# Performance work log

Hardware: AMD Instinct MI355X
Metric: run time of the kernel (lower is better)

The kernel has to match this reference:

```python
import jax, jax.numpy as jnp
import numpy as np

SIDE_LEN = 128
RESOLUTION = 1.0  # Angstrom per pixel


def setup_inputs() -> dict:
    key = jax.random.key(0)
    k1, k2, k3 = jax.random.split(key, 3)
    B, A = 16, 20000
    # atom xyz coords in Angstrom, spread within the field of view (+/- 63.5 A)
    mol = jax.random.normal(k1, (B, A, 3), dtype=jnp.float32) * 20.0
    # per-atom Gaussian std in [0.5, 1.5) A (strictly positive)
    stds = jax.random.uniform(k2, (A,), dtype=jnp.float32) + 0.5
    # per-atom density (mass) in [0.5, 1.5)
    densities = jax.random.uniform(k3, (A,), dtype=jnp.float32) + 0.5
    return {"mol": mol, "stds": stds, "densities": densities}


def reference(mol, stds, densities):
    # Pixel-center coordinate grid, identical to torch.arange(-x_max, x_max+1e-5, res)
    x_max = (SIDE_LEN - 1) * RESOLUTION / 2
    coord = jnp.arange(-x_max, x_max + 1e-5, RESOLUTION, dtype=jnp.float32)  # (S,)
    var = stds * stds                              # (A,)
    neg_half_inv_var = (-0.5 / var)[None, :, None] # (1,A,1)
    # Separable Gaussian profiles: exp(-(coord - mu)^2 / (2 var))
    dx = coord[None, None, :] - mol[:, :, 0:1]     # (B,A,S) x-offsets
    dy = coord[None, None, :] - mol[:, :, 1:2]     # (B,A,S) y-offsets
    gx = jnp.exp(neg_half_inv_var * dx * dx)       # (B,A,W)
    gy = jnp.exp(neg_half_inv_var * dy * dy)       # (B,A,H)
    coef = densities / (2.0 * jnp.pi * var)        # (A,)
    # img[b,h,w] = sum_a coef_a * gy[b,a,h] * gx[b,a,w]  (batched matmul)
    img = jnp.einsum('bah,baw->bhw', gy * coef[None, :, None], gx)
    return img  # (B, SIDE_LEN, SIDE_LEN)
```

## Files before the change

### kernel.cpp

```cpp
#include <hip/hip_runtime.h>


#define S 128
#define NS 32
#define PER 640
#define BLOCK 1024
#define KC 32
#define GSTR 40

typedef _Float16 f16;
typedef _Float16 f16x2 __attribute__((ext_vector_type(2)));
typedef _Float16 f16x4 __attribute__((ext_vector_type(4)));
typedef _Float16 f16x8 __attribute__((ext_vector_type(8)));
typedef float floatx16 __attribute__((ext_vector_type(16)));

#if __has_builtin(__builtin_amdgcn_exp2f)
#define FAST_EXP2(x) __builtin_amdgcn_exp2f(x)
#else
#define FAST_EXP2(x) exp2f(x)
#endif
#if __has_builtin(__builtin_amdgcn_rcpf)
#define FAST_RCP(x) __builtin_amdgcn_rcpf(x)
#else
#define FAST_RCP(x) (1.0f / (x))
#endif

static __device__ __forceinline__ f16x2 PKRTZ(float a, float b) {
#if __has_builtin(__builtin_amdgcn_cvt_pkrtz)
    return __builtin_bit_cast(f16x2, __builtin_amdgcn_cvt_pkrtz(a, b));
#else
    return (f16x2){(f16)a, (f16)b};
#endif
}

union frag_u { f16x8 v; f16x4 q[2]; f16x2 h[4]; };
union half4_u { f16x4 q; f16x2 h[2]; };

struct SharedT {
    float4 sG[PER];
    f16 g[2][2][S * GSTR];
};

__global__ __launch_bounds__(BLOCK, 8) void k_proj(
    const float* __restrict__ mol,
    const float* __restrict__ stds,
    const float* __restrict__ dens,
    f16* __restrict__ part,
    int B, int A)
{
    __shared__ SharedT sh;

    const int ks   = blockIdx.x;
    const int b    = blockIdx.y;
    const int tid  = threadIdx.x;
    const int lane = tid & 63;
    const int wav  = tid >> 6;
    const int l31  = lane & 31;
    const int hi   = lane >> 5;

    const int a0  = ks * PER;
    const int a1  = min(a0 + PER, A);
    const int cnt = a1 - a0;

    for (int i = tid; i < cnt; i += BLOCK) {
        const int a = a0 + i;
        const size_t idx = (size_t)b * A + a;
        float x  = mol[idx * 3 + 0];
        float y  = mol[idx * 3 + 1];
        float v  = stds[a] * stds[a];
        float rv = FAST_RCP(v);
        float z  = -0.72134752044448f * rv;
        float w  = __log2f(dens[a] * 0.15915494309189535f * rv);
        sh.sG[i] = make_float4(x, y, z, w);
    }
    __syncthreads();

    const int nc = cnt >> 5;

    const int gaxis = wav >> 3;
    const int agrp  = wav & 7;
    const float c0  = (float)lane - 63.5f;

    const int arow = (wav >> 2) * 32 + l31;
    const int bcol = (wav & 3) * 32 + l31;
    const int koff = hi * 8;

    floatx16 acc = (floatx16){0.f};

    auto GEN_COMPUTE = [&](int c, half4_u& V0, half4_u& V1) {
        const float4* prm = &sh.sG[c * KC + agrp * 4];
#pragma unroll
        for (int i2 = 0; i2 < 2; ++i2) {
            float e0[2], e1[2];
#pragma unroll
            for (int u = 0; u < 2; ++u) {
                float4 p = prm[i2 * 2 + u];
                float mu = gaxis ? p.y : p.x;
                float wc = gaxis ? p.w : 0.0f;
                float d  = c0 - mu;
                float t  = p.z * d;
                float g0 = fmaf(t, d, wc);
                float g1 = fmaf(128.0f, t, fmaf(4096.0f, p.z, g0));
                e0[u] = FAST_EXP2(g0);
                e1[u] = FAST_EXP2(g1);
            }
            V0.h[i2] = PKRTZ(e0[0], e0[1]);
            V1.h[i2] = PKRTZ(e1[0], e1[1]);
        }
    };

#define STEP(P)                                                                \
    do {                                                                       \
        const f16* gy = sh.g[(P)][1];                                          \
        const f16* gx = sh.g[(P)][0];                                          \
        const bool gen = (c + 1 < nc);                                         \
        half4_u V0, V1;                                                        \
        if (gen) GEN_COMPUTE(c + 1, V0, V1);                                   \
        _Pragma("unroll")                                                      \
        for (int s = 0; s < 2; ++s) {                                          \
            frag_u Af, Bf;                                                     \
            Af.v = *(const f16x8*)(gy + arow * GSTR + s * 16 + koff);          \
            Bf.v = *(const f16x8*)(gx + bcol * GSTR + s * 16 + koff);          \
            acc = __builtin_amdgcn_mfma_f32_32x32x16_f16(Af.v, Bf.v, acc, 0, 0, 0); \
        }                                                                      \
        if (gen) {                                                             \
            f16* dst = &sh.g[(P) ^ 1][gaxis][lane * GSTR + agrp * 4];          \
            *(f16x4*)dst               = V0.q;                                 \
            *(f16x4*)(dst + 64 * GSTR) = V1.q;                                 \
        }                                                                      \
        __syncthreads();                                                       \
        ++c;                                                                   \
    } while (0)

    {
        half4_u V0, V1;
        GEN_COMPUTE(0, V0, V1);
        f16* dst = &sh.g[0][gaxis][lane * GSTR + agrp * 4];
        *(f16x4*)dst               = V0.q;
        *(f16x4*)(dst + 64 * GSTR) = V1.q;
    }
    __syncthreads();

    int c = 0;
    while (c + 2 <= nc) { STEP(0); STEP(1); }
    if (c < nc) STEP(0);
#undef STEP

    {
        f16* pq = part + ((size_t)(b * NS + ks)) * (S * S)
                       + (size_t)wav * 1024 + lane * 16;
        frag_u lo, hiv;
#pragma unroll
        for (int jp = 0; jp < 4; ++jp) {
            lo.h[jp]  = PKRTZ(acc[2 * jp],     acc[2 * jp + 1]);
            hiv.h[jp] = PKRTZ(acc[2 * jp + 8], acc[2 * jp + 9]);
        }
        *(f16x8*)(pq + 0) = lo.v;
        *(f16x8*)(pq + 8) = hiv.v;
    }
}

__global__ __launch_bounds__(256) void k_reduce(const f16* __restrict__ part,
                                                float* __restrict__ out) {
    __shared__ float lred[3][64][9];
    const int b    = blockIdx.z;
    const int lane = threadIdx.x & 63;
    const int w    = threadIdx.x >> 6;
    const int f8   = (blockIdx.x * 64 + lane) * 8;

    const f16* src = part + (size_t)b * NS * (S * S) + (size_t)(w * 8) * (S * S) + f8;
    float s[8] = {0.f};
#pragma unroll
    for (int t = 0; t < 8; ++t) {
        f16x8 v = *(const f16x8*)&src[(size_t)t * (S * S)];
#pragma unroll
        for (int i = 0; i < 8; ++i) s[i] += (float)v[i];
    }

    if (w) {
#pragma unroll
        for (int i = 0; i < 8; ++i) lred[w - 1][lane][i] = s[i];
    }
    __syncthreads();

    if (w == 0) {
#pragma unroll
        for (int j = 0; j < 3; ++j)
#pragma unroll
            for (int i = 0; i < 8; ++i) s[i] += lred[j][lane][i];

        const int reg0   = f8 & 15;
        const int lane_f = (f8 >> 4) & 63;
        const int tile   = f8 >> 10;
        const int r      = tile >> 2;
        const int cc     = tile & 3;
        const int rowb = r * 32 + 4 * (lane_f >> 5);
        const int col  = cc * 32 + (lane_f & 31);
#pragma unroll
        for (int i = 0; i < 8; ++i) {
            const int reg = reg0 + i;
            const int row = rowb + (reg & 3) + 8 * (reg >> 2);
            out[((size_t)b * S + row) * S + col] = s[i];
        }
    }
}

extern "C" void kernel_launch(void* const* d_in, const int* in_sizes, int n_in,
                              void* d_out, int out_size, void* d_ws, size_t ws_size,
                              hipStream_t stream) {
    const float* mol  = (const float*)d_in[0];
    const float* stds = (const float*)d_in[1];
    const float* dens = (const float*)d_in[2];
    float* out = (float*)d_out;

    const int A = in_sizes[1];
    const int B = in_sizes[0] / (A * 3);

    f16* part = (f16*)d_ws;

    k_proj<<<dim3(NS, B), dim3(BLOCK), 0, stream>>>(mol, stds, dens, part, B, A);
    k_reduce<<<dim3((S * S) / (64 * 8), 1, B), dim3(256), 0, stream>>>(part, out);
}
```

Baseline: 85.65 us.

## Keep per-atom parameters in registers and broadcast via readlane instead of LDS

Removes the LDS staging of per-atom parameters and its prologue barrier. Each wave now loads the parameters for its own atom subset into registers, two chunk sets per lane, and broadcasts them with readlane during Gaussian generation. This cuts LDS footprint and LDS reads. The cost is redundant global loads and log/rcp work across waves, plus scalar readlane traffic. It assumes nc <= 32, which holds since PER is 640 and KC is 32.

```diff
diff --git a/kernel.cpp b/kernel.cpp
--- a/kernel.cpp
+++ b/kernel.cpp
@@ -33,13 +33,13 @@
 #endif
 }
 
+static __device__ __forceinline__ float RDLANE(float v, int sl) {
+    return __builtin_bit_cast(float,
+        __builtin_amdgcn_readlane(__builtin_bit_cast(int, v), sl));
+}
+
 union frag_u { f16x8 v; f16x4 q[2]; f16x2 h[4]; };
 union half4_u { f16x4 q; f16x2 h[2]; };
-
-struct SharedT {
-    float4 sG[PER];
-    f16 g[2][2][S * GSTR];
-};
 
 __global__ __launch_bounds__(BLOCK, 8) void k_proj(
     const float* __restrict__ mol,
@@ -48,7 +48,7 @@
     f16* __restrict__ part,
     int B, int A)
 {
-    __shared__ SharedT sh;
+    __shared__ f16 g[2][2][S * GSTR];
 
     const int ks   = blockIdx.x;
     const int b    = blockIdx.y;
@@ -61,21 +61,7 @@
     const int a0  = ks * PER;
     const int a1  = min(a0 + PER, A);
     const int cnt = a1 - a0;
-
-    for (int i = tid; i < cnt; i += BLOCK) {
-        const int a = a0 + i;
-        const size_t idx = (size_t)b * A + a;
-        float x  = mol[idx * 3 + 0];
-        float y  = mol[idx * 3 + 1];
-        float v  = stds[a] * stds[a];
-        float rv = FAST_RCP(v);
-        float z  = -0.72134752044448f * rv;
-        float w  = __log2f(dens[a] * 0.15915494309189535f * rv);
-        sh.sG[i] = make_float4(x, y, z, w);
-    }
-    __syncthreads();
-
-    const int nc = cnt >> 5;
+    const int nc  = cnt >> 5;
 
     const int gaxis = wav >> 3;
     const int agrp  = wav & 7;
@@ -85,22 +71,41 @@
     const int bcol = (wav & 3) * 32 + l31;
     const int koff = hi * 8;
 
+    float mu0, z0, w0, mu1, z1, w1;
+    {
+        auto LOADP = [&](int c, float& mu, float& z, float& w) {
+            const int cc = min(c, nc - 1);
+            const int a  = a0 + cc * KC + agrp * 4 + (lane & 3);
+            const size_t idx = (size_t)b * A + a;
+            float mx = mol[idx * 3 + 0];
+            float my = mol[idx * 3 + 1];
+            float v  = stds[a] * stds[a];
+            float rv = FAST_RCP(v);
+            z  = -0.72134752044448f * rv;
+            w  = gaxis ? __log2f(dens[a] * 0.15915494309189535f * rv) : 0.0f;
+            mu = gaxis ? my : mx;
+        };
+        LOADP(lane >> 2,        mu0, z0, w0);
+        LOADP(16 + (lane >> 2), mu1, z1, w1);
+    }
+
     floatx16 acc = (floatx16){0.f};
 
-    auto GEN_COMPUTE = [&](int c, half4_u& V0, half4_u& V1) {
-        const float4* prm = &sh.sG[c * KC + agrp * 4];
+    auto GEN_FROM = [&](float muR, float zR, float wR, int lb,
+                        half4_u& V0, half4_u& V1) {
 #pragma unroll
         for (int i2 = 0; i2 < 2; ++i2) {
             float e0[2], e1[2];
 #pragma unroll
             for (int u = 0; u < 2; ++u) {
-                float4 p = prm[i2 * 2 + u];
-                float mu = gaxis ? p.y : p.x;
-                float wc = gaxis ? p.w : 0.0f;
+                const int sl = lb + i2 * 2 + u;
+                float mu = RDLANE(muR, sl);
+                float z  = RDLANE(zR,  sl);
+                float w  = RDLANE(wR,  sl);
                 float d  = c0 - mu;
-                float t  = p.z * d;
-                float g0 = fmaf(t, d, wc);
-                float g1 = fmaf(128.0f, t, fmaf(4096.0f, p.z, g0));
+                float t  = z * d;
+                float g0 = fmaf(t, d, w);
+                float g1 = fmaf(128.0f, t, fmaf(4096.0f, z, g0));
                 e0[u] = FAST_EXP2(g0);
                 e1[u] = FAST_EXP2(g1);
             }
@@ -108,11 +113,15 @@
             V1.h[i2] = PKRTZ(e1[0], e1[1]);
         }
     };
+    auto GEN_COMPUTE = [&](int c, half4_u& V0, half4_u& V1) {
+        if (c < 16) GEN_FROM(mu0, z0, w0, c * 4, V0, V1);
+        else        GEN_FROM(mu1, z1, w1, (c - 16) * 4, V0, V1);
+    };
 
 #define STEP(P)                                                                \
     do {                                                                       \
-        const f16* gy = sh.g[(P)][1];                                          \
-        const f16* gx = sh.g[(P)][0];                                          \
+        const f16* gy = g[(P)][1];                                             \
+        const f16* gx = g[(P)][0];                                             \
         const bool gen = (c + 1 < nc);                                         \
         half4_u V0, V1;                                                        \
         if (gen) GEN_COMPUTE(c + 1, V0, V1);                                   \
@@ -124,7 +133,7 @@
             acc = __builtin_amdgcn_mfma_f32_32x32x16_f16(Af.v, Bf.v, acc, 0, 0, 0); \
         }                                                                      \
         if (gen) {                                                             \
-            f16* dst = &sh.g[(P) ^ 1][gaxis][lane * GSTR + agrp * 4];          \
+            f16* dst = &g[(P) ^ 1][gaxis][lane * GSTR + agrp * 4];             \
             *(f16x4*)dst               = V0.q;                                 \
             *(f16x4*)(dst + 64 * GSTR) = V1.q;                                 \
         }                                                                      \
@@ -135,7 +144,7 @@
     {
         half4_u V0, V1;
         GEN_COMPUTE(0, V0, V1);
-        f16* dst = &sh.g[0][gaxis][lane * GSTR + agrp * 4];
+        f16* dst = &g[0][gaxis][lane * GSTR + agrp * 4];
         *(f16x4*)dst               = V0.q;
         *(f16x4*)(dst + 64 * GSTR) = V1.q;
     }
```

After: 93.19 us. 1.09x slower.

## Split output rows across two blocks with 512-thread blocks and padded LDS

Applied to the files above, without the earlier changes.

The projection kernel now launches two blocks per (slice, batch), each covering 64 output rows, and shrinks blocks to 512 threads. Each wave generates x-profiles for all 128 columns plus y-profiles for its own 64 rows. The LDS row stride changes from 40 to 36 halfs, with fragment loads split into 8-byte reads, to change the bank-conflict pattern. The cost is that every block recomputes the x-profiles and reloads the atom parameters, which duplicates that work across the two halves.

```diff
diff --git a/kernel.cpp b/kernel.cpp
--- a/kernel.cpp
+++ b/kernel.cpp
@@ -4,9 +4,9 @@
 #define S 128
 #define NS 32
 #define PER 640
-#define BLOCK 1024
+#define BLOCK 512
 #define KC 32
-#define GSTR 40
+#define GSTR 36
 
 typedef _Float16 f16;
 typedef _Float16 f16x2 __attribute__((ext_vector_type(2)));
@@ -38,7 +38,8 @@
 
 struct SharedT {
     float4 sG[PER];
-    f16 g[2][2][S * GSTR];
+    f16 gx[2][S * GSTR];
+    f16 gy[2][64 * GSTR];
 };
 
 __global__ __launch_bounds__(BLOCK, 8) void k_proj(
@@ -52,6 +53,7 @@
 
     const int ks   = blockIdx.x;
     const int b    = blockIdx.y;
+    const int h    = blockIdx.z;
     const int tid  = threadIdx.x;
     const int lane = tid & 63;
     const int wav  = tid >> 6;
@@ -61,6 +63,7 @@
     const int a0  = ks * PER;
     const int a1  = min(a0 + PER, A);
     const int cnt = a1 - a0;
+    const int nc  = cnt >> 5;
 
     for (int i = tid; i < cnt; i += BLOCK) {
         const int a = a0 + i;
@@ -75,11 +78,9 @@
     }
     __syncthreads();
 
-    const int nc = cnt >> 5;
-
-    const int gaxis = wav >> 3;
-    const int agrp  = wav & 7;
-    const float c0  = (float)lane - 63.5f;
+    const int agrp  = wav;
+    const float cx0 = (float)lane - 63.5f;
+    const float cy0 = (float)(h * 64 + lane) - 63.5f;
 
     const int arow = (wav >> 2) * 32 + l31;
     const int bcol = (wav & 3) * 32 + l31;
@@ -87,58 +88,58 @@
 
     floatx16 acc = (floatx16){0.f};
 
-    auto GEN_COMPUTE = [&](int c, half4_u& V0, half4_u& V1) {
+    auto GEN_CHUNK = [&](int c, int par) {
         const float4* prm = &sh.sG[c * KC + agrp * 4];
+        half4_u X0, X1, Y0;
 #pragma unroll
         for (int i2 = 0; i2 < 2; ++i2) {
-            float e0[2], e1[2];
+            float ex0[2], ex1[2], ey0[2];
 #pragma unroll
             for (int u = 0; u < 2; ++u) {
                 float4 p = prm[i2 * 2 + u];
-                float mu = gaxis ? p.y : p.x;
-                float wc = gaxis ? p.w : 0.0f;
-                float d  = c0 - mu;
+                float d  = cx0 - p.x;
                 float t  = p.z * d;
-                float g0 = fmaf(t, d, wc);
+                float g0 = t * d;
                 float g1 = fmaf(128.0f, t, fmaf(4096.0f, p.z, g0));
-                e0[u] = FAST_EXP2(g0);
-                e1[u] = FAST_EXP2(g1);
+                ex0[u] = FAST_EXP2(g0);
+                ex1[u] = FAST_EXP2(g1);
+                float dy = cy0 - p.y;
+                float ty = p.z * dy;
+                ey0[u] = FAST_EXP2(fmaf(ty, dy, p.w));
             }
-            V0.h[i2] = PKRTZ(e0[0], e0[1]);
-            V1.h[i2] = PKRTZ(e1[0], e1[1]);
+            X0.h[i2] = PKRTZ(ex0[0], ex0[1]);
+            X1.h[i2] = PKRTZ(ex1[0], ex1[1]);
+            Y0.h[i2] = PKRTZ(ey0[0], ey0[1]);
         }
+        f16* dx = &sh.gx[par][lane * GSTR + agrp * 4];
+        *(f16x4*)dx               = X0.q;
+        *(f16x4*)(dx + 64 * GSTR) = X1.q;
+        f16* dy_ = &sh.gy[par][lane * GSTR + agrp * 4];
+        *(f16x4*)dy_ = Y0.q;
     };
 
 #define STEP(P)                                                                \
     do {                                                                       \
-        const f16* gy = sh.g[(P)][1];                                          \
-        const f16* gx = sh.g[(P)][0];                                          \
+        const f16* gy = sh.gy[(P)];                                            \
+        const f16* gx = sh.gx[(P)];                                            \
         const bool gen = (c + 1 < nc);                                         \
-        half4_u V0, V1;                                                        \
-        if (gen) GEN_COMPUTE(c + 1, V0, V1);                                   \
+        if (gen) GEN_CHUNK(c + 1, (P) ^ 1);                                    \
         _Pragma("unroll")                                                      \
         for (int s = 0; s < 2; ++s) {                                          \
             frag_u Af, Bf;                                                     \
-            Af.v = *(const f16x8*)(gy + arow * GSTR + s * 16 + koff);          \
-            Bf.v = *(const f16x8*)(gx + bcol * GSTR + s * 16 + koff);          \
+            const f16* ay = gy + arow * GSTR + s * 16 + koff;                  \
+            const f16* bx = gx + bcol * GSTR + s * 16 + koff;                  \
+            Af.q[0] = *(const f16x4*)(ay);                                     \
+            Af.q[1] = *(const f16x4*)(ay + 4);                                 \
+            Bf.q[0] = *(const f16x4*)(bx);                                     \
+            Bf.q[1] = *(const f16x4*)(bx + 4);                                 \
             acc = __builtin_amdgcn_mfma_f32_32x32x16_f16(Af.v, Bf.v, acc, 0, 0, 0); \
-        }                                                                      \
-        if (gen) {                                                             \
-            f16* dst = &sh.g[(P) ^ 1][gaxis][lane * GSTR + agrp * 4];          \
-            *(f16x4*)dst               = V0.q;                                 \
-            *(f16x4*)(dst + 64 * GSTR) = V1.q;                                 \
         }                                                                      \
         __syncthreads();                                                       \
         ++c;                                                                   \
     } while (0)
 
-    {
-        half4_u V0, V1;
-        GEN_COMPUTE(0, V0, V1);
-        f16* dst = &sh.g[0][gaxis][lane * GSTR + agrp * 4];
-        *(f16x4*)dst               = V0.q;
-        *(f16x4*)(dst + 64 * GSTR) = V1.q;
-    }
+    GEN_CHUNK(0, 0);
     __syncthreads();
 
     int c = 0;
@@ -147,8 +148,9 @@
 #undef STEP
 
     {
+        const int tileidx = (2 * h + (wav >> 2)) * 4 + (wav & 3);
         f16* pq = part + ((size_t)(b * NS + ks)) * (S * S)
-                       + (size_t)wav * 1024 + lane * 16;
+                       + (size_t)tileidx * 1024 + lane * 16;
         frag_u lo, hiv;
 #pragma unroll
         for (int jp = 0; jp < 4; ++jp) {
@@ -218,6 +220,6 @@
 
     f16* part = (f16*)d_ws;
 
-    k_proj<<<dim3(NS, B), dim3(BLOCK), 0, stream>>>(mol, stds, dens, part, B, A);
+    k_proj<<<dim3(NS, B, 2), dim3(BLOCK), 0, stream>>>(mol, stds, dens, part, B, A);
     k_reduce<<<dim3((S * S) / (64 * 8), 1, B), dim3(256), 0, stream>>>(part, out);
 }
```

Measured after the change: 90.34 us. 1.05x slower.
